# Performance work log

Hardware: AMD Instinct MI355X
Metric: run time of the kernel (lower is better)

## Reference

```python
import jax, jax.numpy as jnp
import numpy as np

B, S, D = 2, 2048, 2048
H, HD = 16, 128          # n_heads, head_dim
RD = 64                  # rope_head_dim
ND = HD - RD             # nope_head_dim = 64
KVR, QR = 512, 1024      # kv_lora_rank, q_lora_rank
BASE = 10000.0
NEG = -1e30


def _apply_rope(t):
    # t: [B, H, S, RD]; GPT-NeoX half-split rotation
    half = RD // 2
    seq = t.shape[2]
    inv_freq = 1.0 / (BASE ** (jnp.arange(half, dtype=jnp.float32) / half))
    ang = jnp.arange(seq, dtype=jnp.float32)[:, None] * inv_freq  # [S, half]
    cos, sin = jnp.cos(ang), jnp.sin(ang)
    t1, t2 = t[..., :half], t[..., half:]
    return jnp.concatenate([t1 * cos - t2 * sin, t1 * sin + t2 * cos], axis=-1)


def setup_inputs() -> dict:
    key = jax.random.key(0)
    ks = jax.random.split(key, 9)
    def w(k, shape):  # weights stored [in, out], so y = x @ W
        return jax.random.normal(k, shape, jnp.float32) * (shape[0] ** -0.5)
    return {
        "x": jax.random.normal(ks[0], (B, S, D), jnp.float32),
        "Wq_down": w(ks[1], (D, QR)),
        "Wq_up": w(ks[2], (QR, H * ND)),
        "Wq_rope": w(ks[3], (QR, H * RD)),
        "Wkv_down": w(ks[4], (D, KVR)),
        "Wk_up": w(ks[5], (KVR, H * ND)),
        "Wk_rope": w(ks[6], (D, H * RD)),
        "Wv_up": w(ks[7], (KVR, H * HD)),
        "Wo": w(ks[8], (H * HD, D)),
    }


def reference(x, Wq_down, Wq_up, Wq_rope, Wkv_down, Wk_up, Wk_rope, Wv_up, Wo):
    b, s, _ = x.shape
    # low-rank query path
    q_lat = x @ Wq_down                                            # [B,S,QR]
    q_nope = (q_lat @ Wq_up).reshape(b, s, H, ND).transpose(0, 2, 1, 3)
    q_pe = (q_lat @ Wq_rope).reshape(b, s, H, RD).transpose(0, 2, 1, 3)
    # low-rank KV path (decoupled rope key comes straight from x)
    kv_lat = x @ Wkv_down                                          # [B,S,KVR]
    k_nope = (kv_lat @ Wk_up).reshape(b, s, H, ND).transpose(0, 2, 1, 3)
    k_pe = (x @ Wk_rope).reshape(b, s, H, RD).transpose(0, 2, 1, 3)
    v = (kv_lat @ Wv_up).reshape(b, s, H, HD).transpose(0, 2, 1, 3)
    # decoupled RoPE on the PE branches only
    q_pe = _apply_rope(q_pe)
    k_pe = _apply_rope(k_pe)
    q = jnp.concatenate([q_nope, q_pe], axis=-1)                   # [B,H,S,HD]
    k = jnp.concatenate([k_nope, k_pe], axis=-1)                   # [B,H,S,HD]
    # causal SDPA (no mask/cache supplied -> is_causal=True)
    scale = HD ** -0.5
    scores = jnp.einsum("bhqd,bhkd->bhqk", q, k) * scale
    causal = jnp.tril(jnp.ones((s, s), dtype=bool))
    scores = jnp.where(causal, scores, NEG)
    attn = jax.nn.softmax(scores, axis=-1)
    out = jnp.einsum("bhqk,bhkd->bhqd", attn, v)
    out = out.transpose(0, 2, 1, 3).reshape(b, s, H * HD)
    return out @ Wo
```

## Files before the change

kernel.cpp:

```cpp
#include <hip/hip_runtime.h>
#include <hip/hip_bf16.h>

typedef unsigned short u16;
typedef short bf16x8 __attribute__((ext_vector_type(8)));
typedef float f32x4 __attribute__((ext_vector_type(4)));

static __device__ __forceinline__ u16 f2b(float f) {
  unsigned u = __float_as_uint(f);
  u += 0x7fffu + ((u >> 16) & 1u);
  return (u16)(u >> 16);
}
static __device__ __forceinline__ float b2f(u16 h) {
  return __uint_as_float(((unsigned)h) << 16);
}
static __device__ __forceinline__ f32x4 mfma16(bf16x8 a, bf16x8 b, f32x4 c) {
  return __builtin_amdgcn_mfma_f32_16x16x32_bf16(a, b, c, 0, 0, 0);
}

__device__ __align__(16) float g_rope[2048][64];

__global__ void rope_fill()
{
  int i = blockIdx.x * 256 + threadIdx.x;
  int s = i >> 5, j = i & 31;
  float invf = __expf(-(float)j * 0.28782313662425575f);
  float ang = (float)s * invf;
  g_rope[s][j] = cosf(ang);
  g_rope[s][32 + j] = sinf(ang);
}

__global__ void conv_f32_bf16(const float* __restrict__ src, u16* __restrict__ dst, int n4)
{
  int stride = gridDim.x * blockDim.x;
  for (int i = blockIdx.x * blockDim.x + threadIdx.x; i < n4; i += stride) {
    float4 v = ((const float4*)src)[i];
    ushort4 o;
    o.x = f2b(v.x); o.y = f2b(v.y); o.z = f2b(v.z); o.w = f2b(v.w);
    ((ushort4*)dst)[i] = o;
  }
}

__global__ void wtrans(const float* __restrict__ src, int K, int N,
                       u16* __restrict__ dst, int dld, int roff)
{
  __shared__ float tile[32][33];
  int n0 = blockIdx.x << 5, k0 = blockIdx.y << 5;
  int tx = threadIdx.x & 31, ty = threadIdx.x >> 5;
  #pragma unroll
  for (int p = 0; p < 4; ++p) {
    int kk = (p << 3) + ty;
    tile[kk][tx] = src[(size_t)(k0 + kk) * N + n0 + tx];
  }
  __syncthreads();
  #pragma unroll
  for (int p = 0; p < 4; ++p) {
    int nn = (p << 3) + ty;
    dst[(size_t)(roff + n0 + nn) * dld + k0 + tx] = f2b(tile[tx][nn]);
  }
}

__global__ __launch_bounds__(256, 2)
void gemm_bt(const u16* __restrict__ A, const u16* __restrict__ Bt,
             void* __restrict__ C, int K, int lda, int ldb, int ldc, int c_f32)
{
  __shared__ u16 As[128 * 64];
  __shared__ u16 Bs[128 * 64];
  const int t = threadIdx.x;
  const int lane = t & 63;
  const int m0 = blockIdx.y << 7, n0 = blockIdx.x << 7;
  const int w = t >> 6;
  const int wm = (w >> 1) << 6;
  const int wn = (w & 1) << 6;
  const int r15 = lane & 15, hi = lane >> 4;

  f32x4 acc[4][4];
  #pragma unroll
  for (int i = 0; i < 4; ++i)
    #pragma unroll
    for (int j = 0; j < 4; ++j)
      acc[i][j] = (f32x4){0.f, 0.f, 0.f, 0.f};

  for (int kt = 0; kt < K; kt += 64) {
    __syncthreads();
    #pragma unroll
    for (int p = 0; p < 4; ++p) {
      int g = (p << 8) + t;
      int row = g >> 3;
      int sl = (g & 7) ^ (row & 7);
      const u16* ga = A + (size_t)(m0 + row) * lda + kt + (sl << 3);
      __builtin_amdgcn_global_load_lds(
          (const __attribute__((address_space(1))) void*)ga,
          (__attribute__((address_space(3))) void*)((char*)As + g * 16), 16, 0, 0);
      const u16* gb = Bt + (size_t)(n0 + row) * ldb + kt + (sl << 3);
      __builtin_amdgcn_global_load_lds(
          (const __attribute__((address_space(1))) void*)gb,
          (__attribute__((address_space(3))) void*)((char*)Bs + g * 16), 16, 0, 0);
    }
    __syncthreads();
    #pragma unroll
    for (int kk = 0; kk < 2; ++kk) {
      int ks = (kk << 2) + hi;
      bf16x8 af[4], bfr[4];
      #pragma unroll
      for (int mi = 0; mi < 4; ++mi) {
        int row = wm + (mi << 4) + r15;
        af[mi] = *(const bf16x8*)((const char*)As + row * 128 + ((ks ^ (row & 7)) << 4));
      }
      #pragma unroll
      for (int ni = 0; ni < 4; ++ni) {
        int row = wn + (ni << 4) + r15;
        bfr[ni] = *(const bf16x8*)((const char*)Bs + row * 128 + ((ks ^ (row & 7)) << 4));
      }
      #pragma unroll
      for (int mi = 0; mi < 4; ++mi)
        #pragma unroll
        for (int ni = 0; ni < 4; ++ni)
          acc[mi][ni] = mfma16(af[mi], bfr[ni], acc[mi][ni]);
    }
  }

  if (c_f32) {
    float* Cf = (float*)C;
    #pragma unroll
    for (int mi = 0; mi < 4; ++mi)
      #pragma unroll
      for (int ni = 0; ni < 4; ++ni) {
        int row = m0 + wm + (mi << 4) + (hi << 2);
        int col = n0 + wn + (ni << 4) + r15;
        #pragma unroll
        for (int r = 0; r < 4; ++r)
          Cf[(size_t)(row + r) * ldc + col] = acc[mi][ni][r];
      }
  } else {
    u16* Cb = (u16*)C;
    #pragma unroll
    for (int mi = 0; mi < 4; ++mi)
      #pragma unroll
      for (int ni = 0; ni < 4; ++ni) {
        int row = m0 + wm + (mi << 4) + (hi << 2);
        int col = n0 + wn + (ni << 4) + r15;
        #pragma unroll
        for (int r = 0; r < 4; ++r)
          Cb[(size_t)(row + r) * ldc + col] = f2b(acc[mi][ni][r]);
      }
  }
}

__global__ void pack_q(const u16* __restrict__ qout, u16* __restrict__ Qb)
{
  int rid = (blockIdx.x << 2) + (threadIdx.x >> 6);
  int lane = threadIdx.x & 63;
  int s = rid & 2047, h = (rid >> 11) & 15;
  int b = rid >> 15;
  const u16* src = qout + (size_t)((b << 11) + s) * 2048;
  const float scale = 0.08838834764831845f;
  float vn = b2f(src[(h << 6) + lane]) * scale;
  int j = lane & 31;
  float t1 = b2f(src[1024 + (h << 6) + j]);
  float t2 = b2f(src[1024 + (h << 6) + 32 + j]);
  float c = g_rope[s][j], sn = g_rope[s][32 + j];
  float vp = (lane < 32) ? (t1 * c - t2 * sn) : (t1 * sn + t2 * c);
  vp *= scale;
  u16* dst = Qb + (size_t)rid * 128;
  dst[lane] = f2b(vn);
  dst[64 + lane] = f2b(vp);
}

__global__ void pack_k(const u16* __restrict__ kvout, const u16* __restrict__ lat1,
                       u16* __restrict__ Kb)
{
  int rid = (blockIdx.x << 2) + (threadIdx.x >> 6);
  int lane = threadIdx.x & 63;
  int s = rid & 2047, h = (rid >> 11) & 15;
  int b = rid >> 15;
  size_t row = (size_t)((b << 11) + s);
  float vn = b2f(kvout[row * 3072 + (h << 6) + lane]);
  int j = lane & 31;
  float t1 = b2f(lat1[row * 2560 + 1536 + (h << 6) + j]);
  float t2 = b2f(lat1[row * 2560 + 1536 + (h << 6) + 32 + j]);
  float c = g_rope[s][j], sn = g_rope[s][32 + j];
  float vp = (lane < 32) ? (t1 * c - t2 * sn) : (t1 * sn + t2 * c);
  u16* dst = Kb + (size_t)rid * 128;
  dst[lane] = f2b(vn);
  dst[64 + lane] = f2b(vp);
}

__global__ void pack_vt(const u16* __restrict__ kvout, u16* __restrict__ Vt)
{
  __shared__ u16 tile[32][33];
  int bi = blockIdx.x;
  int dt = bi & 3, st = (bi >> 2) & 63, h = (bi >> 8) & 15, b = bi >> 12;
  int tx = threadIdx.x & 31, ty = threadIdx.x >> 5;
  #pragma unroll
  for (int p = 0; p < 4; ++p) {
    int s = (st << 5) + (p << 3) + ty;
    tile[(p << 3) + ty][tx] =
        kvout[(size_t)((b << 11) + s) * 3072 + 1024 + (h << 7) + (dt << 5) + tx];
  }
  __syncthreads();
  #pragma unroll
  for (int p = 0; p < 4; ++p) {
    int d = (dt << 5) + (p << 3) + ty;
    Vt[(size_t)(((b << 4) + h) * 128 + d) * 2048 + (st << 5) + tx] = tile[tx][(p << 3) + ty];
  }
}

__global__ __launch_bounds__(512, 4)
void attn_fwd(const u16* __restrict__ Qb, const u16* __restrict__ Kb,
              const u16* __restrict__ Vt, u16* __restrict__ AO)
{
  __shared__ __align__(16) u16 Kl[64 * 128];
  __shared__ __align__(16) u16 Vl[128 * 64];
  __shared__ __align__(16) u16 Pl[8][16 * 72];

  const int S = 2048;
  int g = (int)(blockIdx.x >> 5);
  int qtg = (g < 8) ? (15 - g) : (g - 8);
  int bh = blockIdx.x & 31;
  int b = bh >> 4, h = bh & 15;
  int t = threadIdx.x, lane = t & 63, w = t >> 6;
  int q0 = qtg << 7;
  int qw = q0 + (w << 4);
  int r15 = lane & 15, hi = lane >> 4;

  const u16* Qp = Qb + (size_t)bh * S * 128;
  const u16* Kp = Kb + (size_t)bh * S * 128;
  const u16* Vp = Vt + (size_t)bh * 128 * S;

  bf16x8 qf[4];
  #pragma unroll
  for (int kk = 0; kk < 4; ++kk)
    qf[kk] = *(const bf16x8*)(Qp + (size_t)(qw + r15) * 128 + kk * 32 + hi * 8);

  f32x4 o[8];
  #pragma unroll
  for (int i = 0; i < 8; ++i) o[i] = (f32x4){0.f, 0.f, 0.f, 0.f};
  float mrun[4] = {-1e30f, -1e30f, -1e30f, -1e30f};
  float lrun[4] = {0.f, 0.f, 0.f, 0.f};

  int ntiles = (qtg << 1) + 2;
  for (int kt = 0; kt < ntiles; ++kt) {
    int kv0 = kt << 6;
    __syncthreads();
    #pragma unroll
    for (int p = 0; p < 2; ++p) {
      int gg = t + (p << 9);
      int rk = gg >> 4, ck = gg & 15, sk = ck ^ (rk & 15);
      const u16* ga = Kp + (size_t)(kv0 + rk) * 128 + (sk << 3);
      __builtin_amdgcn_global_load_lds(
          (const __attribute__((address_space(1))) void*)ga,
          (__attribute__((address_space(3))) void*)((char*)Kl + gg * 16), 16, 0, 0);
      int rv = gg >> 3, cv = gg & 7, sv = cv ^ (rv & 7);
      const u16* gv = Vp + (size_t)rv * S + kv0 + (sv << 3);
      __builtin_amdgcn_global_load_lds(
          (const __attribute__((address_space(1))) void*)gv,
          (__attribute__((address_space(3))) void*)((char*)Vl + gg * 16), 16, 0, 0);
    }
    __syncthreads();

    if (kv0 <= qw + 15) {
      f32x4 sc[4];
      __builtin_amdgcn_s_setprio(1);
      #pragma unroll
      for (int nt = 0; nt < 4; ++nt) {
        f32x4 a = (f32x4){0.f, 0.f, 0.f, 0.f};
        int row = (nt << 4) + r15;
        #pragma unroll
        for (int kk = 0; kk < 4; ++kk) {
          int ch = (kk << 2) + hi;
          bf16x8 kf = *(const bf16x8*)((const char*)Kl + row * 256 + ((ch ^ (row & 15)) << 4));
          a = mfma16(qf[kk], kf, a);
        }
        sc[nt] = a;
      }
      __builtin_amdgcn_s_setprio(0);

      bool maskt = (kv0 + 63 > qw);
      float corr[4];
      u16* pw = Pl[w];
      #pragma unroll
      for (int r = 0; r < 4; ++r) {
        float s0 = sc[0][r], s1 = sc[1][r], s2 = sc[2][r], s3 = sc[3][r];
        if (maskt) {
          int qg = qw + (hi << 2) + r;
          int kvc = kv0 + r15;
          s0 = (kvc <= qg) ? s0 : -1e30f;
          s1 = (kvc + 16 <= qg) ? s1 : -1e30f;
          s2 = (kvc + 32 <= qg) ? s2 : -1e30f;
          s3 = (kvc + 48 <= qg) ? s3 : -1e30f;
        }
        float mt = fmaxf(fmaxf(s0, s1), fmaxf(s2, s3));
        #pragma unroll
        for (int off = 1; off < 16; off <<= 1) mt = fmaxf(mt, __shfl_xor(mt, off, 64));
        float mn = fmaxf(mrun[r], mt);
        float cr = __expf(mrun[r] - mn);
        float p0 = __expf(s0 - mn), p1 = __expf(s1 - mn);
        float p2 = __expf(s2 - mn), p3 = __expf(s3 - mn);
        float ps = (p0 + p1) + (p2 + p3);
        #pragma unroll
        for (int off = 1; off < 16; off <<= 1) ps += __shfl_xor(ps, off, 64);
        lrun[r] = lrun[r] * cr + ps;
        mrun[r] = mn;
        corr[r] = cr;
        int prow = (hi << 2) + r;
        pw[prow * 72 + r15]      = f2b(p0);
        pw[prow * 72 + 16 + r15] = f2b(p1);
        pw[prow * 72 + 32 + r15] = f2b(p2);
        pw[prow * 72 + 48 + r15] = f2b(p3);
      }
      #pragma unroll
      for (int dt = 0; dt < 8; ++dt) {
        f32x4 t4 = o[dt];
        t4[0] *= corr[0]; t4[1] *= corr[1]; t4[2] *= corr[2]; t4[3] *= corr[3];
        o[dt] = t4;
      }

      bf16x8 pf[2];
      #pragma unroll
      for (int kk = 0; kk < 2; ++kk)
        pf[kk] = *(const bf16x8*)((const char*)pw + r15 * 144 + (kk << 6) + (hi << 4));
      __builtin_amdgcn_s_setprio(1);
      #pragma unroll
      for (int dt = 0; dt < 8; ++dt) {
        int vrow = (dt << 4) + r15;
        #pragma unroll
        for (int kk = 0; kk < 2; ++kk) {
          int chv = (kk << 2) + hi;
          bf16x8 vf = *(const bf16x8*)((const char*)Vl + vrow * 128 + ((chv ^ (vrow & 7)) << 4));
          o[dt] = mfma16(pf[kk], vf, o[dt]);
        }
      }
      __builtin_amdgcn_s_setprio(0);
    }
  }

  #pragma unroll
  for (int r = 0; r < 4; ++r) {
    float inv = 1.0f / lrun[r];
    size_t rowb = (size_t)(b * 2048 + qw + (hi << 2) + r) * 2048 + h * 128;
    #pragma unroll
    for (int dt = 0; dt < 8; ++dt)
      AO[rowb + dt * 16 + r15] = f2b(o[dt][r] * inv);
  }
}

extern "C" void kernel_launch(void* const* d_in, const int* in_sizes, int n_in,
                              void* d_out, int out_size, void* d_ws, size_t ws_size,
                              hipStream_t stream)
{
  const float* x        = (const float*)d_in[0];
  const float* Wq_down  = (const float*)d_in[1];
  const float* Wq_up    = (const float*)d_in[2];
  const float* Wq_rope  = (const float*)d_in[3];
  const float* Wkv_down = (const float*)d_in[4];
  const float* Wk_up    = (const float*)d_in[5];
  const float* Wk_rope  = (const float*)d_in[6];
  const float* Wv_up    = (const float*)d_in[7];
  const float* Wo       = (const float*)d_in[8];

  char* ws = (char*)d_ws;
  u16* xb    = (u16*)(ws + 0);
  u16* W1t   = (u16*)(ws + 16777216);
  u16* W2t   = (u16*)(ws + 27262976);
  u16* W3t   = (u16*)(ws + 31457280);
  u16* Wot   = (u16*)(ws + 34603008);
  u16* lat1  = (u16*)(ws + 42991616);
  u16* qout  = (u16*)(ws + 63963136);
  u16* kvout = (u16*)(ws + 80740352);
  u16* Qb    = (u16*)(ws + 105906176);
  u16* Kb    = (u16*)(ws + 122683392);
  u16* Vtb   = (u16*)(ws + 139460608);
  u16* AO    = xb;
  if (ws_size < 156237824u) return;

  rope_fill<<<256, 256, 0, stream>>>();
  conv_f32_bf16<<<2048, 256, 0, stream>>>(x, xb, 2097152);

  wtrans<<<dim3(32, 64), 256, 0, stream>>>(Wq_down,  2048, 1024, W1t, 2048, 0);
  wtrans<<<dim3(16, 64), 256, 0, stream>>>(Wkv_down, 2048,  512, W1t, 2048, 1024);
  wtrans<<<dim3(32, 64), 256, 0, stream>>>(Wk_rope,  2048, 1024, W1t, 2048, 1536);
  wtrans<<<dim3(32, 32), 256, 0, stream>>>(Wq_up,    1024, 1024, W2t, 1024, 0);
  wtrans<<<dim3(32, 32), 256, 0, stream>>>(Wq_rope,  1024, 1024, W2t, 1024, 1024);
  wtrans<<<dim3(32, 16), 256, 0, stream>>>(Wk_up,     512, 1024, W3t,  512, 0);
  wtrans<<<dim3(64, 16), 256, 0, stream>>>(Wv_up,     512, 2048, W3t,  512, 1024);
  wtrans<<<dim3(64, 64), 256, 0, stream>>>(Wo,       2048, 2048, Wot, 2048, 0);

  gemm_bt<<<dim3(20, 32), 256, 0, stream>>>(xb, W1t, lat1, 2048, 2048, 2048, 2560, 0);
  gemm_bt<<<dim3(16, 32), 256, 0, stream>>>(lat1, W2t, qout, 1024, 2560, 1024, 2048, 0);
  gemm_bt<<<dim3(24, 32), 256, 0, stream>>>(lat1 + 1024, W3t, kvout, 512, 2560, 512, 3072, 0);

  pack_q<<<16384, 256, 0, stream>>>(qout, Qb);
  pack_k<<<16384, 256, 0, stream>>>(kvout, lat1, Kb);
  pack_vt<<<8192, 256, 0, stream>>>(kvout, Vtb);

  attn_fwd<<<512, 512, 0, stream>>>(Qb, Kb, Vtb, AO);

  gemm_bt<<<dim3(16, 32), 256, 0, stream>>>(AO, Wot, d_out, 2048, 2048, 2048, 2048, 1);

  (void)in_sizes; (void)n_in; (void)out_size;
}
```

Before: 422.9 us.

## Transpose attention MFMA operands so each lane owns one query row

Swaps the A/B operands of the QK and PV MFMAs so the accumulator is transposed and each lane holds a single query row. The softmax then needs one running max/sum per lane with two cross-lane shuffles instead of four, and uses native exp2 with log2(e) folded into the Q scale. P is stored to LDS as packed 8-byte writes with an XOR swizzle in place of a padded layout, and the output is written as vectorized 4-element stores. The aim is to cut shuffle, exp and LDS-store overhead in the inner loop, at the cost of a more intricate indexing scheme that has to stay correct.

```diff
diff --git a/kernel.cpp b/kernel.cpp
--- a/kernel.cpp
+++ b/kernel.cpp
@@ -15,6 +15,9 @@
 }
 static __device__ __forceinline__ f32x4 mfma16(bf16x8 a, bf16x8 b, f32x4 c) {
   return __builtin_amdgcn_mfma_f32_16x16x32_bf16(a, b, c, 0, 0, 0);
+}
+static __device__ __forceinline__ float fexp2(float x) {
+  return __builtin_amdgcn_exp2f(x);
 }
 
 __device__ __align__(16) float g_rope[2048][64];
@@ -153,7 +156,7 @@
   int s = rid & 2047, h = (rid >> 11) & 15;
   int b = rid >> 15;
   const u16* src = qout + (size_t)((b << 11) + s) * 2048;
-  const float scale = 0.08838834764831845f;
+  const float scale = 0.12751743f;
   float vn = b2f(src[(h << 6) + lane]) * scale;
   int j = lane & 31;
   float t1 = b2f(src[1024 + (h << 6) + j]);
@@ -211,7 +214,7 @@
 {
   __shared__ __align__(16) u16 Kl[64 * 128];
   __shared__ __align__(16) u16 Vl[128 * 64];
-  __shared__ __align__(16) u16 Pl[8][16 * 72];
+  __shared__ __align__(16) u16 Pl[8][16 * 64];
 
   const int S = 2048;
   int g = (int)(blockIdx.x >> 5);
@@ -235,8 +238,10 @@
   f32x4 o[8];
   #pragma unroll
   for (int i = 0; i < 8; ++i) o[i] = (f32x4){0.f, 0.f, 0.f, 0.f};
-  float mrun[4] = {-1e30f, -1e30f, -1e30f, -1e30f};
-  float lrun[4] = {0.f, 0.f, 0.f, 0.f};
+  float mrun = -1e30f, lrun = 0.f;
+
+  int qme = qw + r15;
+  u16* pw = Pl[w];
 
   int ntiles = (qtg << 1) + 2;
   for (int kt = 0; kt < ntiles; ++kt) {
@@ -269,78 +274,93 @@
         for (int kk = 0; kk < 4; ++kk) {
           int ch = (kk << 2) + hi;
           bf16x8 kf = *(const bf16x8*)((const char*)Kl + row * 256 + ((ch ^ (row & 15)) << 4));
-          a = mfma16(qf[kk], kf, a);
+          a = mfma16(kf, qf[kk], a);
         }
         sc[nt] = a;
       }
       __builtin_amdgcn_s_setprio(0);
 
-      bool maskt = (kv0 + 63 > qw);
-      float corr[4];
-      u16* pw = Pl[w];
-      #pragma unroll
-      for (int r = 0; r < 4; ++r) {
-        float s0 = sc[0][r], s1 = sc[1][r], s2 = sc[2][r], s3 = sc[3][r];
-        if (maskt) {
-          int qg = qw + (hi << 2) + r;
-          int kvc = kv0 + r15;
-          s0 = (kvc <= qg) ? s0 : -1e30f;
-          s1 = (kvc + 16 <= qg) ? s1 : -1e30f;
-          s2 = (kvc + 32 <= qg) ? s2 : -1e30f;
-          s3 = (kvc + 48 <= qg) ? s3 : -1e30f;
+      if (kv0 + 63 > qw) {
+        #pragma unroll
+        for (int nt = 0; nt < 4; ++nt) {
+          int kvb = kv0 + (nt << 4) + (hi << 2);
+          #pragma unroll
+          for (int r = 0; r < 4; ++r)
+            sc[nt][r] = (kvb + r <= qme) ? sc[nt][r] : -1e30f;
         }
-        float mt = fmaxf(fmaxf(s0, s1), fmaxf(s2, s3));
-        #pragma unroll
-        for (int off = 1; off < 16; off <<= 1) mt = fmaxf(mt, __shfl_xor(mt, off, 64));
-        float mn = fmaxf(mrun[r], mt);
-        float cr = __expf(mrun[r] - mn);
-        float p0 = __expf(s0 - mn), p1 = __expf(s1 - mn);
-        float p2 = __expf(s2 - mn), p3 = __expf(s3 - mn);
-        float ps = (p0 + p1) + (p2 + p3);
-        #pragma unroll
-        for (int off = 1; off < 16; off <<= 1) ps += __shfl_xor(ps, off, 64);
-        lrun[r] = lrun[r] * cr + ps;
-        mrun[r] = mn;
-        corr[r] = cr;
-        int prow = (hi << 2) + r;
-        pw[prow * 72 + r15]      = f2b(p0);
-        pw[prow * 72 + 16 + r15] = f2b(p1);
-        pw[prow * 72 + 32 + r15] = f2b(p2);
-        pw[prow * 72 + 48 + r15] = f2b(p3);
-      }
+      }
+
+      f32x4 mx = sc[0];
+      #pragma unroll
+      for (int nt = 1; nt < 4; ++nt) {
+        mx[0] = fmaxf(mx[0], sc[nt][0]); mx[1] = fmaxf(mx[1], sc[nt][1]);
+        mx[2] = fmaxf(mx[2], sc[nt][2]); mx[3] = fmaxf(mx[3], sc[nt][3]);
+      }
+      float mt = fmaxf(fmaxf(mx[0], mx[1]), fmaxf(mx[2], mx[3]));
+      mt = fmaxf(mt, __shfl_xor(mt, 16, 64));
+      mt = fmaxf(mt, __shfl_xor(mt, 32, 64));
+      float mn = fmaxf(mrun, mt);
+      float cr = fexp2(mrun - mn);
+      float ps = 0.f;
+      #pragma unroll
+      for (int nt = 0; nt < 4; ++nt) {
+        #pragma unroll
+        for (int r = 0; r < 4; ++r) {
+          float pv = fexp2(sc[nt][r] - mn);
+          sc[nt][r] = pv;
+          ps += pv;
+        }
+      }
+      ps += __shfl_xor(ps, 16, 64);
+      ps += __shfl_xor(ps, 32, 64);
+      lrun = lrun * cr + ps;
+      mrun = mn;
+
       #pragma unroll
       for (int dt = 0; dt < 8; ++dt) {
         f32x4 t4 = o[dt];
-        t4[0] *= corr[0]; t4[1] *= corr[1]; t4[2] *= corr[2]; t4[3] *= corr[3];
+        t4[0] *= cr; t4[1] *= cr; t4[2] *= cr; t4[3] *= cr;
         o[dt] = t4;
       }
 
+      #pragma unroll
+      for (int nt = 0; nt < 4; ++nt) {
+        ushort4 pk;
+        pk.x = f2b(sc[nt][0]); pk.y = f2b(sc[nt][1]);
+        pk.z = f2b(sc[nt][2]); pk.w = f2b(sc[nt][3]);
+        int chunk = ((nt << 1) + (hi >> 1)) ^ (r15 & 7);
+        *(ushort4*)((char*)pw + r15 * 128 + (chunk << 4) + ((hi & 1) << 3)) = pk;
+      }
+
       bf16x8 pf[2];
       #pragma unroll
-      for (int kk = 0; kk < 2; ++kk)
-        pf[kk] = *(const bf16x8*)((const char*)pw + r15 * 144 + (kk << 6) + (hi << 4));
+      for (int m = 0; m < 2; ++m) {
+        int chunk = ((m << 2) + hi) ^ (r15 & 7);
+        pf[m] = *(const bf16x8*)((const char*)pw + r15 * 128 + (chunk << 4));
+      }
       __builtin_amdgcn_s_setprio(1);
       #pragma unroll
       for (int dt = 0; dt < 8; ++dt) {
         int vrow = (dt << 4) + r15;
         #pragma unroll
-        for (int kk = 0; kk < 2; ++kk) {
-          int chv = (kk << 2) + hi;
+        for (int m = 0; m < 2; ++m) {
+          int chv = (m << 2) + hi;
           bf16x8 vf = *(const bf16x8*)((const char*)Vl + vrow * 128 + ((chv ^ (vrow & 7)) << 4));
-          o[dt] = mfma16(pf[kk], vf, o[dt]);
+          o[dt] = mfma16(vf, pf[m], o[dt]);
         }
       }
       __builtin_amdgcn_s_setprio(0);
     }
   }
 
-  #pragma unroll
-  for (int r = 0; r < 4; ++r) {
-    float inv = 1.0f / lrun[r];
-    size_t rowb = (size_t)(b * 2048 + qw + (hi << 2) + r) * 2048 + h * 128;
-    #pragma unroll
-    for (int dt = 0; dt < 8; ++dt)
-      AO[rowb + dt * 16 + r15] = f2b(o[dt][r] * inv);
+  float inv = 1.0f / lrun;
+  size_t rowb = (size_t)(b * 2048 + qw + r15) * 2048 + h * 128 + (hi << 2);
+  #pragma unroll
+  for (int dt = 0; dt < 8; ++dt) {
+    ushort4 ov;
+    ov.x = f2b(o[dt][0] * inv); ov.y = f2b(o[dt][1] * inv);
+    ov.z = f2b(o[dt][2] * inv); ov.w = f2b(o[dt][3] * inv);
+    *(ushort4*)(AO + rowb + (dt << 4)) = ov;
   }
 }
 
```

Result: faster. 389.5 us (-7.9%).
